# Performance work log

Measured on AMD Instinct MI355X. Metric: run time of the kernel, lower is better.

Reference implementation:

```python
import jax, jax.numpy as jnp
import numpy as np
import math

B, T, D, H = 4, 2048, 1024, 8
DK = D // H


def _rel_shift(x):
    # x: [B, H, T, P] with P = 2T-1 (Transformer-XL relative shift)
    b, h, q, p = x.shape
    x = jnp.pad(x, ((0, 0), (0, 0), (0, 0), (1, 0)))
    x = x.reshape(b, h, p + 1, q)[:, :, 1:]
    return x.reshape(b, h, q, p)


def setup_inputs() -> dict:
    key = jax.random.key(0)
    ks = jax.random.split(key, 9)
    s = 0.02
    x = jax.random.normal(ks[0], (B, T, D), jnp.float32)
    pos_emb = jax.random.normal(ks[1], (1, 2 * T - 1, D), jnp.float32)
    Wq = jax.random.normal(ks[2], (D, D), jnp.float32) * s
    Wk = jax.random.normal(ks[3], (D, D), jnp.float32) * s
    Wv = jax.random.normal(ks[4], (D, D), jnp.float32) * s
    Wo = jax.random.normal(ks[5], (D, D), jnp.float32) * s
    Wp = jax.random.normal(ks[6], (D, D), jnp.float32) * s
    pos_bias_u = jax.random.normal(ks[7], (H, DK), jnp.float32) * s
    pos_bias_v = jax.random.normal(ks[8], (H, DK), jnp.float32) * s
    return {"x": x, "pos_emb": pos_emb, "Wq": Wq, "Wk": Wk, "Wv": Wv,
            "Wo": Wo, "Wp": Wp, "pos_bias_u": pos_bias_u, "pos_bias_v": pos_bias_v}


def reference(x, pos_emb, Wq, Wk, Wv, Wo, Wp, pos_bias_u, pos_bias_v):
    b, t, d = x.shape
    h, dk = pos_bias_u.shape
    inv_sdk = 1.0 / math.sqrt(dk)
    # projections (torch Linear: y = x @ W.T)
    q = (x @ Wq.T).reshape(b, t, h, dk)          # [B,T,H,DK]
    k = (x @ Wk.T).reshape(b, t, h, dk)          # [B,T,H,DK]
    v = (x @ Wv.T).reshape(b, t, h, dk)          # [B,T,H,DK]
    p = (pos_emb @ Wp.T).reshape(-1, h, dk)      # [P,H,DK], P = 2T-1
    # content and position scores
    matrix_ac = jnp.einsum('bqhd,bkhd->bhqk', q + pos_bias_u, k)   # [B,H,T,T]
    matrix_bd = jnp.einsum('bqhd,phd->bhqp', q + pos_bias_v, p)    # [B,H,T,2T-1]
    matrix_bd = _rel_shift(matrix_bd)[..., :t]                     # [B,H,T,T]
    scores = (matrix_ac + matrix_bd) * inv_sdk
    attn = jax.nn.softmax(scores, axis=-1)
    out = jnp.einsum('bhqk,bkhd->bqhd', attn, v).reshape(b, t, h * dk)
    return out @ Wo.T
```

## Files before the change

### kernel.cpp

```cpp
#include <hip/hip_runtime.h>
#include <cstdint>
#include <math.h>

#define B_   4
#define T_   2048
#define D_   1024
#define H_   8
#define DK_  128
#define P_   4095
#define PS_  4096

typedef unsigned short ushort_t;
typedef __attribute__((ext_vector_type(8))) short short8;
typedef __attribute__((ext_vector_type(4))) float floatx4;

__device__ inline float bf2f(ushort_t s) {
    return __uint_as_float(((unsigned int)s) << 16);
}
__device__ inline ushort_t f2bf(float f) {
    unsigned int u = __float_as_uint(f);
    u += 0x7fffu + ((u >> 16) & 1u);
    return (ushort_t)(u >> 16);
}

__device__ inline floatx4 mfma16(short8 a, short8 b, floatx4 c) {
    return __builtin_amdgcn_mfma_f32_16x16x32_bf16(a, b, c, 0, 0, 0);
}

__device__ inline void gload_lds16(const ushort_t* g, ushort_t* l) {
    __builtin_amdgcn_global_load_lds(
        (const __attribute__((address_space(1))) unsigned int*)g,
        (__attribute__((address_space(3))) unsigned int*)l, 16, 0, 0);
}

__device__ inline float rowmax16(float x) {
    int t;
    t = __builtin_amdgcn_update_dpp(0, __float_as_int(x), 0x128, 0xf, 0xf, true);
    x = fmaxf(x, __int_as_float(t));
    t = __builtin_amdgcn_update_dpp(0, __float_as_int(x), 0x124, 0xf, 0xf, true);
    x = fmaxf(x, __int_as_float(t));
    t = __builtin_amdgcn_update_dpp(0, __float_as_int(x), 0x4E, 0xf, 0xf, true);
    x = fmaxf(x, __int_as_float(t));
    t = __builtin_amdgcn_update_dpp(0, __float_as_int(x), 0xB1, 0xf, 0xf, true);
    x = fmaxf(x, __int_as_float(t));
    return x;
}

__global__ void detect_kernel(const ushort_t* x, int* flag) {
    if (blockIdx.x == 0 && threadIdx.x == 0) {
        int m = 0;
        for (int i = 0; i < 64; ++i) {
            float v = bf2f(x[2 * i]);
            float a = fabsf(v);
            if (!(a == 0.0f || (a > 1e-20f && a < 1e10f))) m = 1;
        }
        flag[0] = m;
    }
}

#define CV_TOT 17826816
template <int MODE>
__global__ __launch_bounds__(256) void convert_kernel(
    const int* __restrict__ flag,
    const void* __restrict__ x, const void* __restrict__ pe,
    const void* __restrict__ wq, const void* __restrict__ wk,
    const void* __restrict__ wv, const void* __restrict__ wo,
    const void* __restrict__ wp, const void* __restrict__ ub,
    const void* __restrict__ vb, ushort_t* __restrict__ dst)
{
    if (flag[0] != MODE) return;
    const size_t i = ((size_t)blockIdx.x * 256 + threadIdx.x) * 4;
    if (i >= CV_TOT) return;
    const void* s; size_t off;
    if (i < 8388608)       { s = x;  off = i; }
    else if (i < 12581888) { s = pe; off = i - 8388608; }
    else if (i < 13630464) { s = wq; off = i - 12581888; }
    else if (i < 14679040) { s = wk; off = i - 13630464; }
    else if (i < 15727616) { s = wv; off = i - 14679040; }
    else if (i < 16776192) { s = wo; off = i - 15727616; }
    else if (i < 17824768) { s = wp; off = i - 16776192; }
    else if (i < 17825792) { s = ub; off = i - 17824768; }
    else                   { s = vb; off = i - 17825792; }
    const size_t d = i + (i >= 12581888 ? 1024 : 0);
    if (MODE == 0) {
        *(uint2*)(dst + d) = *(const uint2*)((const ushort_t*)s + off);
    } else {
        float4 f = *(const float4*)((const float*)s + off);
        uint2 o;
        o.x = (unsigned)f2bf(f.x) | ((unsigned)f2bf(f.y) << 16);
        o.y = (unsigned)f2bf(f.z) | ((unsigned)f2bf(f.w) << 16);
        *(uint2*)(dst + d) = o;
    }
}

__global__ __launch_bounds__(256, 3) void gemm_mfma(
    const int* __restrict__ flag,
    const ushort_t* __restrict__ A, const ushort_t* __restrict__ W,
    void* __restrict__ C, int smode)
{
    if (smode == 3 && flag[0] != 0) return;
    if (smode == 4 && flag[0] != 1) return;
    const int K = 1024, N = 1024;

    __shared__ ushort_t Al[16 * 512];
    __shared__ ushort_t Wl[16 * 512];

    const int tid  = threadIdx.x;
    const int w    = tid >> 6, lane = tid & 63;
    const int r15  = lane & 15, quad = lane >> 4;
    const int wm   = w >> 1, wn = w & 1;
    const int m0   = blockIdx.y * 128, n0 = blockIdx.x * 128;

    floatx4 acc[4][4];
    const floatx4 z4 = {0.f, 0.f, 0.f, 0.f};
#pragma unroll
    for (int mt = 0; mt < 4; ++mt)
#pragma unroll
        for (int nt = 0; nt < 4; ++nt) acc[mt][nt] = z4;

    for (int k0 = 0; k0 < K; k0 += 64) {
#pragma unroll
        for (int ss = 0; ss < 4; ++ss) {
            const int s  = w * 4 + ss;
            const int mg = s >> 1, ks = s & 1;
            const int row = mg * 16 + r15;
            const int col = k0 + ks * 32 + quad * 8;
            gload_lds16(A + (size_t)(m0 + row) * K + col, &Al[s * 512]);
            gload_lds16(W + (size_t)(n0 + row) * K + col, &Wl[s * 512]);
        }
        __syncthreads();

        short8 af[2][4], bf[2][4];
#pragma unroll
        for (int ks = 0; ks < 2; ++ks) {
#pragma unroll
            for (int mt = 0; mt < 4; ++mt)
                af[ks][mt] = *(const short8*)&Al[(((wm * 4 + mt) * 2 + ks) * 64 + lane) * 8];
#pragma unroll
            for (int nt = 0; nt < 4; ++nt)
                bf[ks][nt] = *(const short8*)&Wl[(((wn * 4 + nt) * 2 + ks) * 64 + lane) * 8];
        }
#pragma unroll
        for (int ks = 0; ks < 2; ++ks)
#pragma unroll
            for (int mt = 0; mt < 4; ++mt)
#pragma unroll
                for (int nt = 0; nt < 4; ++nt)
                    acc[mt][nt] = mfma16(af[ks][mt], bf[ks][nt], acc[mt][nt]);
        __syncthreads();
    }

#pragma unroll
    for (int mt = 0; mt < 4; ++mt)
#pragma unroll
        for (int nt = 0; nt < 4; ++nt)
#pragma unroll
            for (int i = 0; i < 4; ++i) {
                const int m = m0 + wm * 64 + mt * 16 + quad * 4 + i;
                const int n = n0 + wn * 64 + nt * 16 + r15;
                const float v = acc[mt][nt][i];
                if (smode == 0) {
                    const int b = m >> 11, t = m & (T_ - 1);
                    const int h = n >> 7, dk = n & (DK_ - 1);
                    ((ushort_t*)C)[(((size_t)(b * H_ + h)) * T_ + t) * DK_ + dk] = f2bf(v);
                } else if (smode == 1) {
                    const int h = n >> 7, dk = n & (DK_ - 1);
                    ((ushort_t*)C)[((size_t)h * PS_ + m) * DK_ + dk] = f2bf(v);
                } else if (smode == 2) {
                    const int b = m >> 11, t = m & (T_ - 1);
                    const int h = n >> 7, dk = n & (DK_ - 1);
                    ((ushort_t*)C)[((size_t)(b * H_ + h) * DK_ + dk) * T_ + t] = f2bf(v);
                } else if (smode == 3) {
                    ((ushort_t*)C)[(size_t)m * N + n] = f2bf(v);
                } else if (smode == 4) {
                    ((float*)C)[(size_t)m * N + n] = v;
                } else {
                    const int b = m >> 11, t = m & (T_ - 1);
                    const int nn = n & 1023;
                    const int h = nn >> 7, dk = nn & (DK_ - 1);
                    const int wsel = n >> 10;
                    size_t idx;
                    if (wsel == 2)
                        idx = (size_t)16777216 + ((size_t)(b * H_ + h) * DK_ + dk) * T_ + t;
                    else
                        idx = (size_t)wsel * 8388608 +
                              (((size_t)(b * H_ + h)) * T_ + t) * DK_ + dk;
                    ((ushort_t*)C)[idx] = f2bf(v);
                }
            }
}

__global__ __launch_bounds__(256, 2) void attn_mfma(
    const ushort_t* __restrict__ qg,
    const ushort_t* __restrict__ kgl,
    const ushort_t* __restrict__ vt,
    const ushort_t* __restrict__ pg,
    const ushort_t* __restrict__ ubb,
    const ushort_t* __restrict__ vbb,
    ushort_t* __restrict__ ao)
{
    __shared__ ushort_t K_lds[16 * 512];
    __shared__ ushort_t V_lds[16 * 512];
    __shared__ ushort_t P_lds[32 * 512];
    __shared__ __align__(16) ushort_t pr_lds[4][1024];

    const int tid  = threadIdx.x;
    const int w    = tid >> 6;
    const int lane = tid & 63;
    const int r15  = lane & 15;
    const int quad = lane >> 4;

    const int lin  = (int)(blockIdx.y * 32 + blockIdx.x);
    const int swz  = (lin & 7) * 128 + (lin >> 3);
    const int bh   = swz >> 5;
    const int h    = bh & (H_ - 1);
    const int b    = bh >> 3;
    const int q0b  = (swz & 31) * 64;
    const int q0w  = q0b + w * 16;

    short8 quA[4], qvA[4];
    {
        const ushort_t* qrow = qg + ((size_t)bh * T_ + q0w + r15) * DK_;
#pragma unroll
        for (int ks = 0; ks < 4; ++ks) {
            const int dk0 = ks * 32 + quad * 8;
            uint4 q4 = *(const uint4*)(qrow + dk0);
            uint4 u4 = *(const uint4*)(ubb + (size_t)h * DK_ + dk0);
            uint4 v4 = *(const uint4*)(vbb + (size_t)h * DK_ + dk0);
            const ushort_t* qs = (const ushort_t*)&q4;
            const ushort_t* us = (const ushort_t*)&u4;
            const ushort_t* vs = (const ushort_t*)&v4;
#pragma unroll
            for (int j = 0; j < 8; ++j) {
                const float qf = bf2f(qs[j]);
                quA[ks][j] = (short)f2bf(qf + bf2f(us[j]));
                qvA[ks][j] = (short)f2bf(qf + bf2f(vs[j]));
            }
        }
    }

    int src[4], hi[4];
#pragma unroll
    for (int i = 0; i < 4; ++i) {
        const int c = r15 + 15 - quad * 4 - i;
        src[i] = quad * 16 + (c & 15);
        hi[i]  = c >> 4;
    }

    floatx4 o[8];
    const floatx4 z4 = {0.f, 0.f, 0.f, 0.f};
#pragma unroll
    for (int g = 0; g < 8; ++g) o[g] = z4;
    floatx4 lacc = z4;
    float mrun[4];
#pragma unroll
    for (int i = 0; i < 4; ++i) mrun[i] = -1e30f;

    short8 ones8;
#pragma unroll
    for (int j = 0; j < 8; ++j) ones8[j] = (short)0x3F80;

    const float scale = 0.08838834764831845f;

    for (int kc0 = 0; kc0 < T_; kc0 += 64) {
        const int pbb = kc0 - q0b + 1984;

#pragma unroll
        for (int ss = 0; ss < 4; ++ss) {
            const int ck = w * 4 + ss;
            gload_lds16(kgl + ((size_t)bh * T_ + kc0 + w * 16 + r15) * DK_ + ss * 32 + quad * 8,
                        &K_lds[ck * 512]);
            const int cv = w * 4 + ss;
            const int og = cv >> 1, ks2 = cv & 1;
            gload_lds16(vt + ((size_t)(bh * DK_ + og * 16 + r15)) * T_ + kc0 + ks2 * 32 + quad * 8,
                        &V_lds[cv * 512]);
        }
#pragma unroll
        for (int ss = 0; ss < 8; ++ss) {
            const int cp = w * 8 + ss;
            const int gb = cp >> 2, ks = cp & 3;
            gload_lds16(pg + ((size_t)h * PS_ + pbb + gb * 16 + r15) * DK_ + ks * 32 + quad * 8,
                        &P_lds[cp * 512]);
        }
        __syncthreads();

        floatx4 ac[4];
#pragma unroll
        for (int g = 0; g < 4; ++g) {
            ac[g] = z4;
#pragma unroll
            for (int ks = 0; ks < 4; ++ks)
                ac[g] = mfma16(quA[ks],
                               *(const short8*)&K_lds[((g * 4 + ks) * 64 + lane) * 8],
                               ac[g]);
        }
        floatx4 bd[5];
#pragma unroll
        for (int g = 0; g < 5; ++g) {
            bd[g] = z4;
            const int gb = (3 - w) + g;
#pragma unroll
            for (int ks = 0; ks < 4; ++ks)
                bd[g] = mfma16(qvA[ks],
                               *(const short8*)&P_lds[((gb * 4 + ks) * 64 + lane) * 8],
                               bd[g]);
        }

        float pr[4][4];
        float mc[4];
#pragma unroll
        for (int i = 0; i < 4; ++i) {
            float mm = -1e30f;
#pragma unroll
            for (int g = 0; g < 4; ++g) {
                const float lo = __shfl(bd[g][i],     src[i], 64);
                const float hh = __shfl(bd[g + 1][i], src[i], 64);
                const float s  = (ac[g][i] + (hi[i] ? hh : lo)) * scale;
                pr[g][i] = s;
                mm = fmaxf(mm, s);
            }
            mc[i] = rowmax16(mm);
        }
        const bool nd = (mc[0] > mrun[0]) | (mc[1] > mrun[1]) |
                        (mc[2] > mrun[2]) | (mc[3] > mrun[3]);
        if (__any(nd)) {
            float alpha[4];
#pragma unroll
            for (int i = 0; i < 4; ++i) {
                const float mn = fmaxf(mrun[i], mc[i]);
                alpha[i] = __expf(mrun[i] - mn);
                mrun[i] = mn;
            }
#pragma unroll
            for (int g = 0; g < 8; ++g)
#pragma unroll
                for (int i = 0; i < 4; ++i) o[g][i] *= alpha[i];
#pragma unroll
            for (int i = 0; i < 4; ++i) lacc[i] *= alpha[i];
        }
#pragma unroll
        for (int g = 0; g < 4; ++g)
#pragma unroll
            for (int i = 0; i < 4; ++i)
                pr[g][i] = __expf(pr[g][i] - mrun[i]);

#pragma unroll
        for (int g = 0; g < 4; ++g) {
            const int unit = (g >> 1) * 4 + (g & 1) * 2 + (r15 >> 3);
#pragma unroll
            for (int i = 0; i < 4; ++i)
                pr_lds[w][(unit * 16 + quad * 4 + i) * 8 + (r15 & 7)] = f2bf(pr[g][i]);
        }
        short8 pa[2];
#pragma unroll
        for (int ks2 = 0; ks2 < 2; ++ks2)
            pa[ks2] = *(const short8*)&pr_lds[w][(ks2 * 64 + lane) * 8];

#pragma unroll
        for (int og = 0; og < 8; ++og)
#pragma unroll
            for (int ks2 = 0; ks2 < 2; ++ks2)
                o[og] = mfma16(pa[ks2],
                               *(const short8*)&V_lds[((og * 2 + ks2) * 64 + lane) * 8],
                               o[og]);
        lacc = mfma16(pa[0], ones8, lacc);
        lacc = mfma16(pa[1], ones8, lacc);
        __syncthreads();
    }

    float inv[4];
#pragma unroll
    for (int i = 0; i < 4; ++i) inv[i] = 1.0f / lacc[i];
#pragma unroll
    for (int og = 0; og < 8; ++og)
#pragma unroll
        for (int i = 0; i < 4; ++i) {
            const size_t idx =
                ((size_t)(b * T_ + q0w + quad * 4 + i)) * D_ + h * DK_ + og * 16 + r15;
            ao[idx] = f2bf(o[og][i] * inv[i]);
        }
}

extern "C" void kernel_launch(void* const* d_in, const int* in_sizes, int n_in,
                              void* d_out, int out_size, void* d_ws, size_t ws_size,
                              hipStream_t stream) {
    const void* x  = d_in[0];
    const void* pe = d_in[1];
    const void* Wq = d_in[2];
    const void* Wk = d_in[3];
    const void* Wv = d_in[4];
    const void* Wo = d_in[5];
    const void* Wp = d_in[6];
    const void* ub = d_in[7];
    const void* vb = d_in[8];

    int* flag = (int*)d_ws;
    ushort_t* arena = (ushort_t*)d_ws + 16;
    ushort_t* xb   = arena;
    ushort_t* peb  = arena + 8388608;
    ushort_t* wqb  = arena + 12582912;
    ushort_t* wkb  = wqb + 1048576;
    ushort_t* wvb  = wkb + 1048576;
    ushort_t* wob  = wvb + 1048576;
    ushort_t* wpb  = wob + 1048576;
    ushort_t* ubb  = arena + 17825792;
    ushort_t* vbb  = ubb + 1024;
    ushort_t* q_ws  = arena + 17827840;
    ushort_t* k_ws  = q_ws + 8388608;
    ushort_t* vt_ws = k_ws + 8388608;
    ushort_t* p_ws  = vt_ws + 8388608;
    ushort_t* ao_ws = xb;

    detect_kernel<<<1, 64, 0, stream>>>((const ushort_t*)x, flag);

    const int cvb = CV_TOT / 4 / 256;
    convert_kernel<0><<<cvb, 256, 0, stream>>>(flag, x, pe, Wq, Wk, Wv, Wo, Wp, ub, vb, arena);
    convert_kernel<1><<<cvb, 256, 0, stream>>>(flag, x, pe, Wq, Wk, Wv, Wo, Wp, ub, vb, arena);

    gemm_mfma<<<dim3(24, 64), 256, 0, stream>>>(flag, xb, wqb, q_ws, 5);
    gemm_mfma<<<dim3(8, 32), 256, 0, stream>>>(flag, peb, wpb, p_ws, 1);

    attn_mfma<<<dim3(T_ / 64, B_ * H_), 256, 0, stream>>>(
        q_ws, k_ws, vt_ws, p_ws, ubb, vbb, ao_ws);

    const dim3 gX(8, 64);
    gemm_mfma<<<gX, 256, 0, stream>>>(flag, ao_ws, wob, d_out, 3);
    gemm_mfma<<<gX, 256, 0, stream>>>(flag, ao_ws, wob, d_out, 4);
}
```

Baseline: 585.6 us.

## Reuse overlapping positional tiles via LDS ring buffer; merge dtype-dispatch launches

In the attention kernel, the positional-embedding window for each 64-key step overlaps the previous step's window by half. The P tile in LDS becomes an 8-slot ring, and only the 4 new 16-row groups are loaded per iteration after the first, which halves P global loads. Separately, the dtype-specialised convert and output GEMM kernel pairs are merged into single launches that branch on the runtime flag, removing two early-exit launches. The ring logic depends on the loads and the slot rotation staying consistent with the barrier ordering.

```diff
diff --git a/kernel.cpp b/kernel.cpp
--- a/kernel.cpp
+++ b/kernel.cpp
@@ -59,7 +59,6 @@
 }
 
 #define CV_TOT 17826816
-template <int MODE>
 __global__ __launch_bounds__(256) void convert_kernel(
     const int* __restrict__ flag,
     const void* __restrict__ x, const void* __restrict__ pe,
@@ -68,7 +67,6 @@
     const void* __restrict__ wp, const void* __restrict__ ub,
     const void* __restrict__ vb, ushort_t* __restrict__ dst)
 {
-    if (flag[0] != MODE) return;
     const size_t i = ((size_t)blockIdx.x * 256 + threadIdx.x) * 4;
     if (i >= CV_TOT) return;
     const void* s; size_t off;
@@ -82,7 +80,7 @@
     else if (i < 17825792) { s = ub; off = i - 17824768; }
     else                   { s = vb; off = i - 17825792; }
     const size_t d = i + (i >= 12581888 ? 1024 : 0);
-    if (MODE == 0) {
+    if (flag[0] == 0) {
         *(uint2*)(dst + d) = *(const uint2*)((const ushort_t*)s + off);
     } else {
         float4 f = *(const float4*)((const float*)s + off);
@@ -98,8 +96,7 @@
     const ushort_t* __restrict__ A, const ushort_t* __restrict__ W,
     void* __restrict__ C, int smode)
 {
-    if (smode == 3 && flag[0] != 0) return;
-    if (smode == 4 && flag[0] != 1) return;
+    const int fl = flag[0];
     const int K = 1024, N = 1024;
 
     __shared__ ushort_t Al[16 * 512];
@@ -170,10 +167,11 @@
                     const int b = m >> 11, t = m & (T_ - 1);
                     const int h = n >> 7, dk = n & (DK_ - 1);
                     ((ushort_t*)C)[((size_t)(b * H_ + h) * DK_ + dk) * T_ + t] = f2bf(v);
-                } else if (smode == 3) {
-                    ((ushort_t*)C)[(size_t)m * N + n] = f2bf(v);
-                } else if (smode == 4) {
-                    ((float*)C)[(size_t)m * N + n] = v;
+                } else if (smode == 6) {
+                    if (fl == 0)
+                        ((ushort_t*)C)[(size_t)m * N + n] = f2bf(v);
+                    else
+                        ((float*)C)[(size_t)m * N + n] = v;
                 } else {
                     const int b = m >> 11, t = m & (T_ - 1);
                     const int nn = n & 1023;
@@ -262,7 +260,11 @@
 
     const float scale = 0.08838834764831845f;
 
-    for (int kc0 = 0; kc0 < T_; kc0 += 64) {
+    int pring = (124 - (q0b >> 4)) & 7;
+
+    const int NT = T_ / 64;
+    for (int n = 0; n < NT; ++n) {
+        const int kc0 = n * 64;
         const int pbb = kc0 - q0b + 1984;
 
 #pragma unroll
@@ -275,12 +277,24 @@
             gload_lds16(vt + ((size_t)(bh * DK_ + og * 16 + r15)) * T_ + kc0 + ks2 * 32 + quad * 8,
                         &V_lds[cv * 512]);
         }
-#pragma unroll
-        for (int ss = 0; ss < 8; ++ss) {
-            const int cp = w * 8 + ss;
-            const int gb = cp >> 2, ks = cp & 3;
-            gload_lds16(pg + ((size_t)h * PS_ + pbb + gb * 16 + r15) * DK_ + ks * 32 + quad * 8,
-                        &P_lds[cp * 512]);
+        if (n == 0) {
+#pragma unroll
+            for (int ss = 0; ss < 8; ++ss) {
+                const int cp = w * 8 + ss;
+                const int glog = cp >> 2, ks = cp & 3;
+                const int slot = (glog + pring) & 7;
+                gload_lds16(pg + ((size_t)h * PS_ + pbb + glog * 16 + r15) * DK_ + ks * 32 + quad * 8,
+                            &P_lds[(slot * 4 + ks) * 512]);
+            }
+        } else {
+#pragma unroll
+            for (int ss = 0; ss < 4; ++ss) {
+                const int cp = w * 4 + ss;
+                const int glog = 4 + (cp >> 2), ks = cp & 3;
+                const int slot = (glog + pring) & 7;
+                gload_lds16(pg + ((size_t)h * PS_ + pbb + glog * 16 + r15) * DK_ + ks * 32 + quad * 8,
+                            &P_lds[(slot * 4 + ks) * 512]);
+            }
         }
         __syncthreads();
 
@@ -298,11 +312,11 @@
 #pragma unroll
         for (int g = 0; g < 5; ++g) {
             bd[g] = z4;
-            const int gb = (3 - w) + g;
+            const int slot = ((3 - w) + g + pring) & 7;
 #pragma unroll
             for (int ks = 0; ks < 4; ++ks)
                 bd[g] = mfma16(qvA[ks],
-                               *(const short8*)&P_lds[((gb * 4 + ks) * 64 + lane) * 8],
+                               *(const short8*)&P_lds[((slot * 4 + ks) * 64 + lane) * 8],
                                bd[g]);
         }
 
@@ -366,6 +380,7 @@
         lacc = mfma16(pa[0], ones8, lacc);
         lacc = mfma16(pa[1], ones8, lacc);
         __syncthreads();
+        pring = (pring + 4) & 7;
     }
 
     float inv[4];
@@ -414,8 +429,7 @@
     detect_kernel<<<1, 64, 0, stream>>>((const ushort_t*)x, flag);
 
     const int cvb = CV_TOT / 4 / 256;
-    convert_kernel<0><<<cvb, 256, 0, stream>>>(flag, x, pe, Wq, Wk, Wv, Wo, Wp, ub, vb, arena);
-    convert_kernel<1><<<cvb, 256, 0, stream>>>(flag, x, pe, Wq, Wk, Wv, Wo, Wp, ub, vb, arena);
+    convert_kernel<<<cvb, 256, 0, stream>>>(flag, x, pe, Wq, Wk, Wv, Wo, Wp, ub, vb, arena);
 
     gemm_mfma<<<dim3(24, 64), 256, 0, stream>>>(flag, xb, wqb, q_ws, 5);
     gemm_mfma<<<dim3(8, 32), 256, 0, stream>>>(flag, peb, wpb, p_ws, 1);
@@ -423,7 +437,5 @@
     attn_mfma<<<dim3(T_ / 64, B_ * H_), 256, 0, stream>>>(
         q_ws, k_ws, vt_ws, p_ws, ubb, vbb, ao_ws);
 
-    const dim3 gX(8, 64);
-    gemm_mfma<<<gX, 256, 0, stream>>>(flag, ao_ws, wob, d_out, 3);
-    gemm_mfma<<<gX, 256, 0, stream>>>(flag, ao_ws, wob, d_out, 4);
-}
+    gemm_mfma<<<dim3(8, 64), 256, 0, stream>>>(flag, ao_ws, wob, d_out, 6);
+}
```

Result: faster. 555.5 us (-5.1%).
